# Kernel optimization log

Measured on AMD Instinct MI355X. Metric: run time of the kernel, lower is better.

The kernel has to match this reference:

```python
import jax, jax.numpy as jnp
import numpy as np

N, E, H, C = 10000, 160000, 7, 64
NEG_SLOPE = 0.2


def setup_inputs() -> dict:
    key = jax.random.key(0)
    ks = iter(jax.random.split(key, 32))
    def w(shape, fan_in):
        return jax.random.normal(next(ks), shape, jnp.float32) * (1.0 / np.sqrt(fan_in))
    inp = {
        "x": jax.random.normal(next(ks), (N, 1024), jnp.float32),
        "edge_index": jax.random.randint(next(ks), (2, E), 0, N, jnp.int64),
        # input MLP 1024->512->256->64
        "W1": w((1024, 512), 1024), "b1": jnp.zeros((512,), jnp.float32),
        "W2": w((512, 256), 512),   "b2": jnp.zeros((256,), jnp.float32),
        "W3": w((256, 64), 256),    "b3": jnp.zeros((64,), jnp.float32),
        # 5 stacked GATv2Conv(64,64,heads=7,concat=False) layers
        "Wl": w((5, 64, H * C), 64), "bl": jnp.zeros((5, H * C), jnp.float32),
        "Wr": w((5, 64, H * C), 64),
        "att": w((5, H, C), C),
        "cbias": jnp.zeros((5, C), jnp.float32),
        # output MLP 64->32->16->9
        "V1": w((64, 32), 64), "c1": jnp.zeros((32,), jnp.float32),
        "V2": w((32, 16), 32), "c2": jnp.zeros((16,), jnp.float32),
        "V3": w((16, 9), 16),  "c3": jnp.zeros((9,), jnp.float32),
    }
    return inp


def _gatv2_conv(x, src, dst, Wl, bl, Wr, att, bias):
    # x: [N,64]; src/dst: [E'] (self-loops already appended)
    xl = (x @ Wl + bl).reshape(N, H, C)   # lin_l (with bias)
    xr = (x @ Wr).reshape(N, H, C)        # lin_r (no bias)
    e = jax.nn.leaky_relu(xl[src] + xr[dst], NEG_SLOPE)      # [E',H,C]
    logits = jnp.einsum('ehc,hc->eh', e, att)                # [E',H]
    m = jax.ops.segment_max(logits, dst, num_segments=N)     # [N,H]
    a = jnp.exp(logits - m[dst])
    s = jax.ops.segment_sum(a, dst, num_segments=N)          # [N,H]
    alpha = a / (s[dst] + 1e-16)                             # ragged softmax per dst node
    out = jax.ops.segment_sum(alpha[:, :, None] * xl[src], dst, num_segments=N)  # [N,H,C]
    return out.mean(axis=1) + bias                           # concat=False -> mean heads


def reference(x, edge_index, W1, b1, W2, b2, W3, b3, Wl, bl, Wr, att, cbias,
              V1, c1, V2, c2, V3, c3):
    # GATv2Conv adds self-loops by default
    loops = jnp.arange(N, dtype=edge_index.dtype)
    src = jnp.concatenate([edge_index[0], loops])
    dst = jnp.concatenate([edge_index[1], loops])

    h = jax.nn.relu(x @ W1 + b1)
    h = jax.nn.relu(h @ W2 + b2)
    h = jax.nn.relu(h @ W3 + b3)
    for l in range(5):
        h = jax.nn.relu(_gatv2_conv(h, src, dst, Wl[l], bl[l], Wr[l], att[l], cbias[l]))
    h = jax.nn.relu(h) @ V1 + c1
    h = jax.nn.relu(h) @ V2 + c2
    h = jax.nn.relu(h) @ V3 + c3
    return jax.nn.log_softmax(h, axis=1)
```

## Files before the change

kernel.cpp:

```cpp
#include <hip/hip_runtime.h>
#include <hip/hip_bf16.h>
#include <math.h>

#define NNODES 10000
#define NEDGES 160000
#define ETOT (NEDGES + NNODES)
#define HEADS 7
#define CH 64
#define HC 448
#define HCP 1024

typedef __attribute__((ext_vector_type(8))) short short8;
typedef __attribute__((ext_vector_type(4))) float floatx4;

__device__ __forceinline__ float bf_lo(unsigned u) {
  return __uint_as_float(u << 16);
}
__device__ __forceinline__ float bf_hi(unsigned u) {
  return __uint_as_float(u & 0xffff0000u);
}

__global__ __launch_bounds__(256) void convert_f32_bf16(
    const float* __restrict__ in, short* __restrict__ out, int n4) {
  int i = blockIdx.x * 256 + threadIdx.x;
  if (i < n4) {
    float4 v = *(const float4*)&in[(size_t)i * 4];
    short4 o;
    o.x = __bfloat16_as_short(__float2bfloat16(v.x));
    o.y = __bfloat16_as_short(__float2bfloat16(v.y));
    o.z = __bfloat16_as_short(__float2bfloat16(v.z));
    o.w = __bfloat16_as_short(__float2bfloat16(v.w));
    *(short4*)&out[(size_t)i * 4] = o;
  }
}

__global__ __launch_bounds__(256) void transpose_bf16(
    const float* __restrict__ in, short* __restrict__ out, int K, int N) {
  int idx = blockIdx.x * 256 + threadIdx.x;
  if (idx < K * N) {
    int n = idx / K, k = idx % K;
    out[idx] = __bfloat16_as_short(__float2bfloat16(in[(size_t)k * N + n]));
  }
}

__global__ __launch_bounds__(256) void pack_gat(
    const float* __restrict__ Wl, const float* __restrict__ Wr,
    const float* __restrict__ bl, short* __restrict__ Wgt,
    float* __restrict__ bg) {
  int idx = blockIdx.x * 256 + threadIdx.x;
  if (idx < 5 * HCP * 64) {
    int l = idx / (HCP * 64);
    int rem = idx % (HCP * 64);
    int col = rem / 64, k = rem % 64;
    int half = col >> 9;
    int within = col & 511;
    int c = within >> 3, h = within & 7;
    float v = 0.f;
    if (h < 7) {
      const float* W = half ? Wr : Wl;
      v = W[((size_t)l * 64 + k) * HC + h * 64 + c];
    }
    Wgt[idx] = __bfloat16_as_short(__float2bfloat16(v));
  }
  if (idx < 5 * HCP) {
    int l = idx >> 10, col = idx & 1023;
    int half = col >> 9, within = col & 511;
    int c = within >> 3, h = within & 7;
    bg[idx] = (!half && h < 7) ? bl[(size_t)l * HC + h * 64 + c] : 0.f;
  }
}

template <int BM, int BN, int RELU>
__global__ __launch_bounds__(256) void mfma_gemm(
    const short* __restrict__ A, const short* __restrict__ Bt,
    const float* __restrict__ bias, short* __restrict__ C,
    int M, int K, int Nc) {
  __shared__ short As[BM * 64];
  __shared__ short Bs[BN * 64];
  constexpr int MI = BM / 32;
  constexpr int NJ = BN / 32;
  int tid = threadIdx.x;
  int lane = tid & 63, wave = tid >> 6;
  int wm = wave >> 1, wn = wave & 1;
  int row0 = blockIdx.x * BM, col0 = blockIdx.y * BN;
  floatx4 acc[MI][NJ] = {};

  for (int k0 = 0; k0 < K; k0 += 64) {
    #pragma unroll
    for (int i = 0; i < BM / 32; ++i) {
      int c = i * 4 + wave;
      int r = c * 8 + (lane >> 3);
      int k = (lane & 7) * 8;
      int grow = row0 + r;
      if (grow >= M) grow = M - 1;
      __builtin_amdgcn_global_load_lds(
          (const __attribute__((address_space(1))) void*)(A + (size_t)grow * K + k0 + k),
          (__attribute__((address_space(3))) void*)(As + c * 512), 16, 0, 0);
    }
    #pragma unroll
    for (int i = 0; i < BN / 32; ++i) {
      int c = i * 4 + wave;
      int r = c * 8 + (lane >> 3);
      int k = (lane & 7) * 8;
      int gcol = col0 + r;
      if (gcol >= Nc) gcol = Nc - 1;
      __builtin_amdgcn_global_load_lds(
          (const __attribute__((address_space(1))) void*)(Bt + (size_t)gcol * K + k0 + k),
          (__attribute__((address_space(3))) void*)(Bs + c * 512), 16, 0, 0);
    }
    __syncthreads();
    int lr = lane & 15, lq = lane >> 4;
    #pragma unroll
    for (int kk = 0; kk < 64; kk += 32) {
      short8 af[MI], bf[NJ];
      #pragma unroll
      for (int i = 0; i < MI; ++i)
        af[i] = *(const short8*)&As[(wm * (BM / 2) + i * 16 + lr) * 64 + kk + lq * 8];
      #pragma unroll
      for (int j = 0; j < NJ; ++j)
        bf[j] = *(const short8*)&Bs[(wn * (BN / 2) + j * 16 + lr) * 64 + kk + lq * 8];
      #pragma unroll
      for (int i = 0; i < MI; ++i)
        #pragma unroll
        for (int j = 0; j < NJ; ++j)
          acc[i][j] = __builtin_amdgcn_mfma_f32_16x16x32_bf16(
              af[i], bf[j], acc[i][j], 0, 0, 0);
    }
    __syncthreads();
  }

  int lr = lane & 15, lq = lane >> 4;
  #pragma unroll
  for (int j = 0; j < NJ; ++j) {
    int col = col0 + wn * (BN / 2) + j * 16 + lr;
    float bj = bias ? bias[col] : 0.f;
    #pragma unroll
    for (int i = 0; i < MI; ++i) {
      int rbase = row0 + wm * (BM / 2) + i * 16 + lq * 4;
      #pragma unroll
      for (int r = 0; r < 4; ++r) {
        int row = rbase + r;
        if (row < M) {
          float v = acc[i][j][r] + bj;
          if (RELU) v = fmaxf(v, 0.f);
          C[(size_t)row * Nc + col] = __bfloat16_as_short(__float2bfloat16(v));
        }
      }
    }
  }
}

__global__ void init_cnt(int* __restrict__ cnt) {
  int i = blockIdx.x * 256 + threadIdx.x;
  if (i < NNODES) cnt[i] = 1;
}

__global__ void hist_kernel(const int* __restrict__ ei, int* __restrict__ cnt) {
  int e = blockIdx.x * 256 + threadIdx.x;
  if (e < NEDGES) atomicAdd(&cnt[ei[NEDGES + e]], 1);
}

__global__ __launch_bounds__(1024) void scan_kernel(
    const int* __restrict__ cnt, int* __restrict__ row_start,
    int* __restrict__ cursor) {
  __shared__ int wsum[16];
  int t = threadIdx.x;
  int lane = t & 63, w = t >> 6;
  int base = t * 10;
  int v[10], s = 0;
  #pragma unroll
  for (int i = 0; i < 10; ++i) {
    v[i] = (base + i < NNODES) ? cnt[base + i] : 0;
    s += v[i];
  }
  int incl = s;
  #pragma unroll
  for (int off = 1; off < 64; off <<= 1) {
    int o = __shfl_up(incl, off, 64);
    if (lane >= off) incl += o;
  }
  if (lane == 63) wsum[w] = incl;
  __syncthreads();
  if (w == 0) {
    int wv = (lane < 16) ? wsum[lane] : 0;
    #pragma unroll
    for (int off = 1; off < 16; off <<= 1) {
      int o = __shfl_up(wv, off, 64);
      if (lane >= off) wv += o;
    }
    if (lane < 16) wsum[lane] = wv;
  }
  __syncthreads();
  int woff = (w > 0) ? wsum[w - 1] : 0;
  int excl = woff + incl - s;
  #pragma unroll
  for (int i = 0; i < 10; ++i) {
    if (base + i < NNODES) {
      row_start[base + i] = excl;
      cursor[base + i] = excl;
    }
    excl += v[i];
  }
  if (t == 1023) row_start[NNODES] = wsum[15];
}

__global__ void scatter_self(int* __restrict__ cursor,
                             int* __restrict__ csr_src,
                             int* __restrict__ csr_dst) {
  int n = blockIdx.x * 256 + threadIdx.x;
  if (n < NNODES) {
    int pos = atomicAdd(&cursor[n], 1);
    csr_src[pos] = n;
    csr_dst[pos] = n;
  }
}

__global__ void scatter_kernel(const int* __restrict__ ei,
                               int* __restrict__ cursor,
                               int* __restrict__ csr_src,
                               int* __restrict__ csr_dst) {
  int e = blockIdx.x * 256 + threadIdx.x;
  if (e < NEDGES) {
    int d = ei[NEDGES + e];
    int pos = atomicAdd(&cursor[d], 1);
    csr_src[pos] = ei[e];
    csr_dst[pos] = d;
  }
}

__global__ __launch_bounds__(256) void edge_logits_kernel(
    const short* __restrict__ xlt, const float* __restrict__ att,
    const int* __restrict__ csr_src, const int* __restrict__ csr_dst,
    float* __restrict__ logits) {
  __shared__ float att_s[512];
  for (int i = threadIdx.x; i < 512; i += 256) {
    int c = i >> 3, h = i & 7;
    att_s[i] = (h < 7) ? att[h * 64 + c] : 0.f;
  }
  __syncthreads();
  int lane = threadIdx.x & 63;
  int wid = threadIdx.x >> 6;
  int eo = lane >> 3, cl = lane & 7;
  int e = (blockIdx.x * 4 + wid) * 8 + eo;
  int ec = (e < ETOT) ? e : (ETOT - 1);
  int s = csr_src[ec], d = csr_dst[ec];
  const uint4* xlp = (const uint4*)(xlt + (size_t)s * HCP);
  const uint4* xrp = (const uint4*)(xlt + (size_t)d * HCP + 512);
  float acc[7];
  #pragma unroll
  for (int h = 0; h < 7; ++h) acc[h] = 0.f;
  #pragma unroll
  for (int q = 0; q < 8; ++q) {
    int c = q * 8 + cl;
    uint4 a = xlp[c];
    uint4 b = xrp[c];
    float4 t0 = *(const float4*)&att_s[c * 8];
    float4 t1 = *(const float4*)&att_s[c * 8 + 4];
    float e0 = bf_lo(a.x) + bf_lo(b.x);
    float e1 = bf_hi(a.x) + bf_hi(b.x);
    float e2 = bf_lo(a.y) + bf_lo(b.y);
    float e3 = bf_hi(a.y) + bf_hi(b.y);
    float e4 = bf_lo(a.z) + bf_lo(b.z);
    float e5 = bf_hi(a.z) + bf_hi(b.z);
    float e6 = bf_lo(a.w) + bf_lo(b.w);
    e0 = fmaxf(e0, 0.2f * e0); e1 = fmaxf(e1, 0.2f * e1);
    e2 = fmaxf(e2, 0.2f * e2); e3 = fmaxf(e3, 0.2f * e3);
    e4 = fmaxf(e4, 0.2f * e4); e5 = fmaxf(e5, 0.2f * e5);
    e6 = fmaxf(e6, 0.2f * e6);
    acc[0] += t0.x * e0; acc[1] += t0.y * e1;
    acc[2] += t0.z * e2; acc[3] += t0.w * e3;
    acc[4] += t1.x * e4; acc[5] += t1.y * e5;
    acc[6] += t1.z * e6;
  }
  #pragma unroll
  for (int h = 0; h < 7; ++h) {
    acc[h] += __shfl_xor(acc[h], 1, 64);
    acc[h] += __shfl_xor(acc[h], 2, 64);
    acc[h] += __shfl_xor(acc[h], 4, 64);
  }
  float res = 0.f;
  #pragma unroll
  for (int h = 0; h < 7; ++h) res = (cl == h) ? acc[h] : res;
  if (e < ETOT) logits[(size_t)e * 8 + cl] = res;
}

__global__ __launch_bounds__(256) void gat_agg2_kernel(
    const short* __restrict__ xlt, const float* __restrict__ logits,
    const float* __restrict__ cbias, const int* __restrict__ row_start,
    const int* __restrict__ csr_src, short* __restrict__ hout) {
  __shared__ float alpha_s[4][64];
  int lane = threadIdx.x & 63;
  int wid = threadIdx.x >> 6;
  int n = blockIdx.x * 4 + wid;
  if (n >= NNODES) return;
  int beg = row_start[n], end = row_start[n + 1];

  int eo = lane >> 3, hm = lane & 7;
  float m = -1e30f, ssum = 0.f;
  for (int e = beg + eo; e < end; e += 8) {
    float lg = logits[(size_t)e * 8 + hm];
    float nm = fmaxf(m, lg);
    ssum = ssum * __expf(m - nm) + __expf(lg - nm);
    m = nm;
  }
  #pragma unroll
  for (int st = 8; st <= 32; st <<= 1) {
    float om = __shfl_xor(m, st, 64);
    float os = __shfl_xor(ssum, st, 64);
    float nm = fmaxf(m, om);
    ssum = ssum * __expf(m - nm) + os * __expf(om - nm);
    m = nm;
  }
  float rinv = 1.0f / (ssum + 1e-16f);

  float o0 = 0.f, o1 = 0.f, o2 = 0.f, o3 = 0.f, o4 = 0.f, o5 = 0.f, o6 = 0.f;
  for (int g = beg; g < end; g += 8) {
    int e = g + eo;
    float al = 0.f;
    if (e < end) al = __expf(logits[(size_t)e * 8 + hm] - m) * rinv;
    alpha_s[wid][eo * 8 + hm] = al;
    int lim = end - g;
    if (lim > 8) lim = 8;
    for (int t = 0; t < lim; ++t) {
      int s = csr_src[g + t];
      uint4 xv = *(const uint4*)(xlt + (size_t)s * HCP + lane * 8);
      float4 aA = *(const float4*)&alpha_s[wid][t * 8];
      float4 aB = *(const float4*)&alpha_s[wid][t * 8 + 4];
      o0 += aA.x * bf_lo(xv.x);
      o1 += aA.y * bf_hi(xv.x);
      o2 += aA.z * bf_lo(xv.y);
      o3 += aA.w * bf_hi(xv.y);
      o4 += aB.x * bf_lo(xv.z);
      o5 += aB.y * bf_hi(xv.z);
      o6 += aB.z * bf_lo(xv.w);
    }
  }

  float accv = o0 + o1 + o2 + o3 + o4 + o5 + o6;
  float v = accv * (1.0f / 7.0f) + cbias[lane];
  hout[(size_t)n * 64 + lane] =
      __bfloat16_as_short(__float2bfloat16(fmaxf(v, 0.f)));
}

__global__ __launch_bounds__(256) void out_mlp_kernel(
    const short* __restrict__ h, const float* __restrict__ V1,
    const float* __restrict__ c1, const float* __restrict__ V2,
    const float* __restrict__ c2, const float* __restrict__ V3,
    const float* __restrict__ c3, float* __restrict__ out) {
  __shared__ float hb[4][64], r1[4][32], r2[4][16], z3[4][9];
  int wid = threadIdx.x >> 6;
  int t = threadIdx.x & 63;
  int n = blockIdx.x * 4 + wid;
  hb[wid][t] =
      __uint_as_float(((unsigned)((const unsigned short*)h)[(size_t)n * 64 + t]) << 16);
  __syncthreads();
  if (t < 32) {
    float a = c1[t];
    #pragma unroll
    for (int k = 0; k < 64; ++k) a += hb[wid][k] * V1[k * 32 + t];
    r1[wid][t] = fmaxf(a, 0.f);
  }
  __syncthreads();
  if (t < 16) {
    float a = c2[t];
    #pragma unroll
    for (int k = 0; k < 32; ++k) a += r1[wid][k] * V2[k * 16 + t];
    r2[wid][t] = fmaxf(a, 0.f);
  }
  __syncthreads();
  if (t < 9) {
    float a = c3[t];
    #pragma unroll
    for (int k = 0; k < 16; ++k) a += r2[wid][k] * V3[k * 9 + t];
    z3[wid][t] = a;
  }
  __syncthreads();
  if (t < 9) {
    float mx = z3[wid][0];
    #pragma unroll
    for (int k = 1; k < 9; ++k) mx = fmaxf(mx, z3[wid][k]);
    float s = 0.f;
    #pragma unroll
    for (int k = 0; k < 9; ++k) s += __expf(z3[wid][k] - mx);
    out[(size_t)n * 9 + t] = z3[wid][t] - mx - logf(s);
  }
}

extern "C" void kernel_launch(void* const* d_in, const int* in_sizes, int n_in,
                              void* d_out, int out_size, void* d_ws, size_t ws_size,
                              hipStream_t stream) {
  const float* x   = (const float*)d_in[0];
  const int*   ei  = (const int*)d_in[1];
  const float* W1  = (const float*)d_in[2];
  const float* b1  = (const float*)d_in[3];
  const float* W2  = (const float*)d_in[4];
  const float* b2  = (const float*)d_in[5];
  const float* W3  = (const float*)d_in[6];
  const float* b3  = (const float*)d_in[7];
  const float* Wl  = (const float*)d_in[8];
  const float* bl  = (const float*)d_in[9];
  const float* Wr  = (const float*)d_in[10];
  const float* att = (const float*)d_in[11];
  const float* cb  = (const float*)d_in[12];
  const float* V1  = (const float*)d_in[13];
  const float* c1  = (const float*)d_in[14];
  const float* V2  = (const float*)d_in[15];
  const float* c2  = (const float*)d_in[16];
  const float* V3  = (const float*)d_in[17];
  const float* c3  = (const float*)d_in[18];
  float* out = (float*)d_out;

  char* ws = (char*)d_ws;
  size_t off = 0;
  auto alloc = [&](size_t bytes) {
    void* p = ws + off;
    off = (off + bytes + 255) & ~(size_t)255;
    return p;
  };
  char* region0 = (char*)alloc((size_t)NNODES * 1024 * 2 + 1024);
  short* xb  = (short*)region0;
  short* h2  = (short*)region0;
  short* xlt = (short*)region0;
  char* region1 = (char*)alloc((size_t)NNODES * 512 * 2 + 1024);
  short* h1 = (short*)region1;
  short* hA = (short*)region1;
  short* hB = hA + (size_t)NNODES * 64;
  short* W1t = (short*)alloc((size_t)512 * 1024 * 2);
  short* W2t = (short*)alloc((size_t)256 * 512 * 2);
  short* W3t = (short*)alloc((size_t)64 * 256 * 2);
  short* Wgt = (short*)alloc((size_t)5 * HCP * 64 * 2);
  float* bg  = (float*)alloc((size_t)5 * HCP * 4);
  int* cnt       = (int*)alloc((size_t)NNODES * 4);
  int* row_start = (int*)alloc((size_t)(NNODES + 1) * 4);
  int* cursor    = (int*)alloc((size_t)NNODES * 4);
  int* csr_src   = (int*)alloc((size_t)ETOT * 4);
  int* csr_dst   = (int*)alloc((size_t)ETOT * 4);
  float* logits  = (float*)alloc((size_t)ETOT * 8 * 4);

  convert_f32_bf16<<<(NNODES * 1024 / 4 + 255) / 256, 256, 0, stream>>>(
      x, xb, NNODES * 1024 / 4);
  transpose_bf16<<<(1024 * 512 + 255) / 256, 256, 0, stream>>>(W1, W1t, 1024, 512);
  transpose_bf16<<<(512 * 256 + 255) / 256, 256, 0, stream>>>(W2, W2t, 512, 256);
  transpose_bf16<<<(256 * 64 + 255) / 256, 256, 0, stream>>>(W3, W3t, 256, 64);
  pack_gat<<<(5 * HCP * 64 + 255) / 256, 256, 0, stream>>>(Wl, Wr, bl, Wgt, bg);

  init_cnt<<<(NNODES + 255) / 256, 256, 0, stream>>>(cnt);
  hist_kernel<<<(NEDGES + 255) / 256, 256, 0, stream>>>(ei, cnt);
  scan_kernel<<<1, 1024, 0, stream>>>(cnt, row_start, cursor);
  scatter_self<<<(NNODES + 255) / 256, 256, 0, stream>>>(cursor, csr_src, csr_dst);
  scatter_kernel<<<(NEDGES + 255) / 256, 256, 0, stream>>>(ei, cursor, csr_src, csr_dst);

  mfma_gemm<64, 128, 1><<<dim3(157, 4), 256, 0, stream>>>(
      xb, W1t, b1, h1, NNODES, 1024, 512);
  mfma_gemm<64, 128, 1><<<dim3(157, 2), 256, 0, stream>>>(
      h1, W2t, b2, h2, NNODES, 512, 256);
  mfma_gemm<64, 64, 1><<<dim3(157, 1), 256, 0, stream>>>(
      h2, W3t, b3, hA, NNODES, 256, 64);

  short* hcur = hA;
  short* hnext = hB;
  for (int layer = 0; layer < 5; ++layer) {
    mfma_gemm<128, 128, 0><<<dim3(79, 8), 256, 0, stream>>>(
        hcur, Wgt + (size_t)layer * HCP * 64, bg + (size_t)layer * HCP, xlt,
        NNODES, 64, HCP);
    edge_logits_kernel<<<(ETOT + 31) / 32, 256, 0, stream>>>(
        xlt, att + (size_t)layer * HC, csr_src, csr_dst, logits);
    gat_agg2_kernel<<<2500, 256, 0, stream>>>(
        xlt, logits, cb + (size_t)layer * 64, row_start, csr_src, hnext);
    short* tmp = hcur; hcur = hnext; hnext = tmp;
  }

  out_mlp_kernel<<<2500, 256, 0, stream>>>(hcur, V1, c1, V2, c2, V3, c3, out);
}
```

Before: 576.0 us.

## Fuse GATv2 edge-logit computation into aggregation with online softmax

```diff
diff --git a/kernel.cpp b/kernel.cpp
--- a/kernel.cpp
+++ b/kernel.cpp
@@ -205,125 +205,116 @@
 }
 
 __global__ void scatter_self(int* __restrict__ cursor,
-                             int* __restrict__ csr_src,
-                             int* __restrict__ csr_dst) {
+                             int* __restrict__ csr_src) {
   int n = blockIdx.x * 256 + threadIdx.x;
   if (n < NNODES) {
     int pos = atomicAdd(&cursor[n], 1);
     csr_src[pos] = n;
-    csr_dst[pos] = n;
   }
 }
 
 __global__ void scatter_kernel(const int* __restrict__ ei,
                                int* __restrict__ cursor,
-                               int* __restrict__ csr_src,
-                               int* __restrict__ csr_dst) {
+                               int* __restrict__ csr_src) {
   int e = blockIdx.x * 256 + threadIdx.x;
   if (e < NEDGES) {
     int d = ei[NEDGES + e];
     int pos = atomicAdd(&cursor[d], 1);
     csr_src[pos] = ei[e];
-    csr_dst[pos] = d;
-  }
-}
-
-__global__ __launch_bounds__(256) void edge_logits_kernel(
+  }
+}
+
+__global__ __launch_bounds__(256) void gat_fused_kernel(
     const short* __restrict__ xlt, const float* __restrict__ att,
-    const int* __restrict__ csr_src, const int* __restrict__ csr_dst,
-    float* __restrict__ logits) {
+    const float* __restrict__ cbias, const int* __restrict__ row_start,
+    const int* __restrict__ csr_src, short* __restrict__ hout) {
   __shared__ float att_s[512];
+  __shared__ float alpha_s[4][64];
   for (int i = threadIdx.x; i < 512; i += 256) {
     int c = i >> 3, h = i & 7;
     att_s[i] = (h < 7) ? att[h * 64 + c] : 0.f;
   }
   __syncthreads();
-  int lane = threadIdx.x & 63;
-  int wid = threadIdx.x >> 6;
-  int eo = lane >> 3, cl = lane & 7;
-  int e = (blockIdx.x * 4 + wid) * 8 + eo;
-  int ec = (e < ETOT) ? e : (ETOT - 1);
-  int s = csr_src[ec], d = csr_dst[ec];
-  const uint4* xlp = (const uint4*)(xlt + (size_t)s * HCP);
-  const uint4* xrp = (const uint4*)(xlt + (size_t)d * HCP + 512);
-  float acc[7];
-  #pragma unroll
-  for (int h = 0; h < 7; ++h) acc[h] = 0.f;
-  #pragma unroll
-  for (int q = 0; q < 8; ++q) {
-    int c = q * 8 + cl;
-    uint4 a = xlp[c];
-    uint4 b = xrp[c];
-    float4 t0 = *(const float4*)&att_s[c * 8];
-    float4 t1 = *(const float4*)&att_s[c * 8 + 4];
-    float e0 = bf_lo(a.x) + bf_lo(b.x);
-    float e1 = bf_hi(a.x) + bf_hi(b.x);
-    float e2 = bf_lo(a.y) + bf_lo(b.y);
-    float e3 = bf_hi(a.y) + bf_hi(b.y);
-    float e4 = bf_lo(a.z) + bf_lo(b.z);
-    float e5 = bf_hi(a.z) + bf_hi(b.z);
-    float e6 = bf_lo(a.w) + bf_lo(b.w);
-    e0 = fmaxf(e0, 0.2f * e0); e1 = fmaxf(e1, 0.2f * e1);
-    e2 = fmaxf(e2, 0.2f * e2); e3 = fmaxf(e3, 0.2f * e3);
-    e4 = fmaxf(e4, 0.2f * e4); e5 = fmaxf(e5, 0.2f * e5);
-    e6 = fmaxf(e6, 0.2f * e6);
-    acc[0] += t0.x * e0; acc[1] += t0.y * e1;
-    acc[2] += t0.z * e2; acc[3] += t0.w * e3;
-    acc[4] += t1.x * e4; acc[5] += t1.y * e5;
-    acc[6] += t1.z * e6;
-  }
-  #pragma unroll
-  for (int h = 0; h < 7; ++h) {
-    acc[h] += __shfl_xor(acc[h], 1, 64);
-    acc[h] += __shfl_xor(acc[h], 2, 64);
-    acc[h] += __shfl_xor(acc[h], 4, 64);
-  }
-  float res = 0.f;
-  #pragma unroll
-  for (int h = 0; h < 7; ++h) res = (cl == h) ? acc[h] : res;
-  if (e < ETOT) logits[(size_t)e * 8 + cl] = res;
-}
-
-__global__ __launch_bounds__(256) void gat_agg2_kernel(
-    const short* __restrict__ xlt, const float* __restrict__ logits,
-    const float* __restrict__ cbias, const int* __restrict__ row_start,
-    const int* __restrict__ csr_src, short* __restrict__ hout) {
-  __shared__ float alpha_s[4][64];
   int lane = threadIdx.x & 63;
   int wid = threadIdx.x >> 6;
   int n = blockIdx.x * 4 + wid;
   if (n >= NNODES) return;
   int beg = row_start[n], end = row_start[n + 1];
-
-  int eo = lane >> 3, hm = lane & 7;
-  float m = -1e30f, ssum = 0.f;
-  for (int e = beg + eo; e < end; e += 8) {
-    float lg = logits[(size_t)e * 8 + hm];
-    float nm = fmaxf(m, lg);
-    ssum = ssum * __expf(m - nm) + __expf(lg - nm);
-    m = nm;
-  }
+  int eo = lane >> 3, cl = lane & 7;
+
+  uint4 xr[8];
   #pragma unroll
-  for (int st = 8; st <= 32; st <<= 1) {
-    float om = __shfl_xor(m, st, 64);
-    float os = __shfl_xor(ssum, st, 64);
-    float nm = fmaxf(m, om);
-    ssum = ssum * __expf(m - nm) + os * __expf(om - nm);
-    m = nm;
-  }
-  float rinv = 1.0f / (ssum + 1e-16f);
-
+  for (int q = 0; q < 8; ++q)
+    xr[q] = *(const uint4*)(xlt + (size_t)n * HCP + 512 + (size_t)(q * 8 + cl) * 8);
+
+  float M = -1e30f;
+  float ssum = 0.f;
   float o0 = 0.f, o1 = 0.f, o2 = 0.f, o3 = 0.f, o4 = 0.f, o5 = 0.f, o6 = 0.f;
+
   for (int g = beg; g < end; g += 8) {
-    int e = g + eo;
-    float al = 0.f;
-    if (e < end) al = __expf(logits[(size_t)e * 8 + hm] - m) * rinv;
-    alpha_s[wid][eo * 8 + hm] = al;
     int lim = end - g;
     if (lim > 8) lim = 8;
+    int e = g + eo;
+    int src = csr_src[(e < end) ? e : (end - 1)];
+
+    float a0 = 0.f, a1 = 0.f, a2 = 0.f, a3 = 0.f, a4 = 0.f, a5 = 0.f, a6 = 0.f;
+    const short* xlp = xlt + (size_t)src * HCP;
+    #pragma unroll
+    for (int q = 0; q < 8; ++q) {
+      int c = q * 8 + cl;
+      uint4 a = *(const uint4*)(xlp + (size_t)c * 8);
+      uint4 b = xr[q];
+      float4 t0 = *(const float4*)&att_s[c * 8];
+      float4 t1 = *(const float4*)&att_s[c * 8 + 4];
+      float e0 = bf_lo(a.x) + bf_lo(b.x);
+      float e1 = bf_hi(a.x) + bf_hi(b.x);
+      float e2 = bf_lo(a.y) + bf_lo(b.y);
+      float e3 = bf_hi(a.y) + bf_hi(b.y);
+      float e4 = bf_lo(a.z) + bf_lo(b.z);
+      float e5 = bf_hi(a.z) + bf_hi(b.z);
+      float e6 = bf_lo(a.w) + bf_lo(b.w);
+      e0 = fmaxf(e0, 0.2f * e0); e1 = fmaxf(e1, 0.2f * e1);
+      e2 = fmaxf(e2, 0.2f * e2); e3 = fmaxf(e3, 0.2f * e3);
+      e4 = fmaxf(e4, 0.2f * e4); e5 = fmaxf(e5, 0.2f * e5);
+      e6 = fmaxf(e6, 0.2f * e6);
+      a0 += t0.x * e0; a1 += t0.y * e1;
+      a2 += t0.z * e2; a3 += t0.w * e3;
+      a4 += t1.x * e4; a5 += t1.y * e5;
+      a6 += t1.z * e6;
+    }
+    #pragma unroll
+    for (int st = 1; st <= 4; st <<= 1) {
+      a0 += __shfl_xor(a0, st, 64); a1 += __shfl_xor(a1, st, 64);
+      a2 += __shfl_xor(a2, st, 64); a3 += __shfl_xor(a3, st, 64);
+      a4 += __shfl_xor(a4, st, 64); a5 += __shfl_xor(a5, st, 64);
+      a6 += __shfl_xor(a6, st, 64);
+    }
+    float lg = -1e30f;
+    lg = (cl == 0) ? a0 : lg; lg = (cl == 1) ? a1 : lg;
+    lg = (cl == 2) ? a2 : lg; lg = (cl == 3) ? a3 : lg;
+    lg = (cl == 4) ? a4 : lg; lg = (cl == 5) ? a5 : lg;
+    lg = (cl == 6) ? a6 : lg;
+    if (eo >= lim) lg = -1e30f;
+
+    float cm = lg;
+    cm = fmaxf(cm, __shfl_xor(cm, 8, 64));
+    cm = fmaxf(cm, __shfl_xor(cm, 16, 64));
+    cm = fmaxf(cm, __shfl_xor(cm, 32, 64));
+    float Mn = fmaxf(M, cm);
+    float sc = __expf(M - Mn);
+    float w = __expf(lg - Mn);
+    M = Mn;
+    ssum = ssum * sc + w;
+    alpha_s[wid][eo * 8 + cl] = w;
+    float s0 = __shfl(sc, 0, 64), s1 = __shfl(sc, 1, 64);
+    float s2 = __shfl(sc, 2, 64), s3 = __shfl(sc, 3, 64);
+    float s4 = __shfl(sc, 4, 64), s5 = __shfl(sc, 5, 64);
+    float s6 = __shfl(sc, 6, 64);
+    o0 *= s0; o1 *= s1; o2 *= s2; o3 *= s3; o4 *= s4; o5 *= s5; o6 *= s6;
+
     for (int t = 0; t < lim; ++t) {
-      int s = csr_src[g + t];
-      uint4 xv = *(const uint4*)(xlt + (size_t)s * HCP + lane * 8);
+      int s = __shfl(src, t * 8, 64);
+      uint4 xv = *(const uint4*)(xlt + (size_t)s * HCP + (size_t)lane * 8);
       float4 aA = *(const float4*)&alpha_s[wid][t * 8];
       float4 aB = *(const float4*)&alpha_s[wid][t * 8 + 4];
       o0 += aA.x * bf_lo(xv.x);
@@ -336,7 +327,15 @@
     }
   }
 
-  float accv = o0 + o1 + o2 + o3 + o4 + o5 + o6;
+  ssum += __shfl_xor(ssum, 8, 64);
+  ssum += __shfl_xor(ssum, 16, 64);
+  ssum += __shfl_xor(ssum, 32, 64);
+  float rinv = 1.0f / (ssum + 1e-16f);
+  float r0 = __shfl(rinv, 0, 64), r1 = __shfl(rinv, 1, 64);
+  float r2 = __shfl(rinv, 2, 64), r3 = __shfl(rinv, 3, 64);
+  float r4 = __shfl(rinv, 4, 64), r5 = __shfl(rinv, 5, 64);
+  float r6 = __shfl(rinv, 6, 64);
+  float accv = o0 * r0 + o1 * r1 + o2 * r2 + o3 * r3 + o4 * r4 + o5 * r5 + o6 * r6;
   float v = accv * (1.0f / 7.0f) + cbias[lane];
   hout[(size_t)n * 64 + lane] =
       __bfloat16_as_short(__float2bfloat16(fmaxf(v, 0.f)));
@@ -434,8 +433,6 @@
   int* row_start = (int*)alloc((size_t)(NNODES + 1) * 4);
   int* cursor    = (int*)alloc((size_t)NNODES * 4);
   int* csr_src   = (int*)alloc((size_t)ETOT * 4);
-  int* csr_dst   = (int*)alloc((size_t)ETOT * 4);
-  float* logits  = (float*)alloc((size_t)ETOT * 8 * 4);
 
   convert_f32_bf16<<<(NNODES * 1024 / 4 + 255) / 256, 256, 0, stream>>>(
       x, xb, NNODES * 1024 / 4);
@@ -447,8 +444,8 @@
   init_cnt<<<(NNODES + 255) / 256, 256, 0, stream>>>(cnt);
   hist_kernel<<<(NEDGES + 255) / 256, 256, 0, stream>>>(ei, cnt);
   scan_kernel<<<1, 1024, 0, stream>>>(cnt, row_start, cursor);
-  scatter_self<<<(NNODES + 255) / 256, 256, 0, stream>>>(cursor, csr_src, csr_dst);
-  scatter_kernel<<<(NEDGES + 255) / 256, 256, 0, stream>>>(ei, cursor, csr_src, csr_dst);
+  scatter_self<<<(NNODES + 255) / 256, 256, 0, stream>>>(cursor, csr_src);
+  scatter_kernel<<<(NEDGES + 255) / 256, 256, 0, stream>>>(ei, cursor, csr_src);
 
   mfma_gemm<64, 128, 1><<<dim3(157, 4), 256, 0, stream>>>(
       xb, W1t, b1, h1, NNODES, 1024, 512);
@@ -463,10 +460,9 @@
     mfma_gemm<128, 128, 0><<<dim3(79, 8), 256, 0, stream>>>(
         hcur, Wgt + (size_t)layer * HCP * 64, bg + (size_t)layer * HCP, xlt,
         NNODES, 64, HCP);
-    edge_logits_kernel<<<(ETOT + 31) / 32, 256, 0, stream>>>(
-        xlt, att + (size_t)layer * HC, csr_src, csr_dst, logits);
-    gat_agg2_kernel<<<2500, 256, 0, stream>>>(
-        xlt, logits, cb + (size_t)layer * 64, row_start, csr_src, hnext);
+    gat_fused_kernel<<<2500, 256, 0, stream>>>(
+        xlt, att + (size_t)layer * HC, cb + (size_t)layer * 64,
+        row_start, csr_src, hnext);
     short* tmp = hcur; hcur = hnext; hnext = tmp;
   }
 
```

Result: slower. 661.7 us (+14.9%).

## Drop max-subtraction in softmax, exponentiate logits in edge kernel and fuse normalization

Applied to the files above, without the earlier changes.

```diff
diff --git a/kernel.cpp b/kernel.cpp
--- a/kernel.cpp
+++ b/kernel.cpp
@@ -231,7 +231,7 @@
 __global__ __launch_bounds__(256) void edge_logits_kernel(
     const short* __restrict__ xlt, const float* __restrict__ att,
     const int* __restrict__ csr_src, const int* __restrict__ csr_dst,
-    float* __restrict__ logits) {
+    float* __restrict__ wbuf) {
   __shared__ float att_s[512];
   for (int i = threadIdx.x; i < 512; i += 256) {
     int c = i >> 3, h = i & 7;
@@ -281,62 +281,42 @@
   float res = 0.f;
   #pragma unroll
   for (int h = 0; h < 7; ++h) res = (cl == h) ? acc[h] : res;
-  if (e < ETOT) logits[(size_t)e * 8 + cl] = res;
+  float wv = (cl < 7) ? __expf(res) : 0.f;
+  if (e < ETOT) wbuf[(size_t)e * 8 + cl] = wv;
 }
 
 __global__ __launch_bounds__(256) void gat_agg2_kernel(
-    const short* __restrict__ xlt, const float* __restrict__ logits,
+    const short* __restrict__ xlt, const float* __restrict__ wbuf,
     const float* __restrict__ cbias, const int* __restrict__ row_start,
     const int* __restrict__ csr_src, short* __restrict__ hout) {
-  __shared__ float alpha_s[4][64];
   int lane = threadIdx.x & 63;
   int wid = threadIdx.x >> 6;
   int n = blockIdx.x * 4 + wid;
   if (n >= NNODES) return;
   int beg = row_start[n], end = row_start[n + 1];
 
-  int eo = lane >> 3, hm = lane & 7;
-  float m = -1e30f, ssum = 0.f;
-  for (int e = beg + eo; e < end; e += 8) {
-    float lg = logits[(size_t)e * 8 + hm];
-    float nm = fmaxf(m, lg);
-    ssum = ssum * __expf(m - nm) + __expf(lg - nm);
-    m = nm;
-  }
-  #pragma unroll
-  for (int st = 8; st <= 32; st <<= 1) {
-    float om = __shfl_xor(m, st, 64);
-    float os = __shfl_xor(ssum, st, 64);
-    float nm = fmaxf(m, om);
-    ssum = ssum * __expf(m - nm) + os * __expf(om - nm);
-    m = nm;
-  }
-  float rinv = 1.0f / (ssum + 1e-16f);
-
   float o0 = 0.f, o1 = 0.f, o2 = 0.f, o3 = 0.f, o4 = 0.f, o5 = 0.f, o6 = 0.f;
-  for (int g = beg; g < end; g += 8) {
-    int e = g + eo;
-    float al = 0.f;
-    if (e < end) al = __expf(logits[(size_t)e * 8 + hm] - m) * rinv;
-    alpha_s[wid][eo * 8 + hm] = al;
-    int lim = end - g;
-    if (lim > 8) lim = 8;
-    for (int t = 0; t < lim; ++t) {
-      int s = csr_src[g + t];
-      uint4 xv = *(const uint4*)(xlt + (size_t)s * HCP + lane * 8);
-      float4 aA = *(const float4*)&alpha_s[wid][t * 8];
-      float4 aB = *(const float4*)&alpha_s[wid][t * 8 + 4];
-      o0 += aA.x * bf_lo(xv.x);
-      o1 += aA.y * bf_hi(xv.x);
-      o2 += aA.z * bf_lo(xv.y);
-      o3 += aA.w * bf_hi(xv.y);
-      o4 += aB.x * bf_lo(xv.z);
-      o5 += aB.y * bf_hi(xv.z);
-      o6 += aB.z * bf_lo(xv.w);
-    }
-  }
-
-  float accv = o0 + o1 + o2 + o3 + o4 + o5 + o6;
+  float s0 = 0.f, s1 = 0.f, s2 = 0.f, s3 = 0.f, s4 = 0.f, s5 = 0.f, s6 = 0.f;
+  #pragma unroll 2
+  for (int e = beg; e < end; ++e) {
+    int src = csr_src[e];
+    float4 wa = *(const float4*)&wbuf[(size_t)e * 8];
+    float4 wb = *(const float4*)&wbuf[(size_t)e * 8 + 4];
+    uint4 xv = *(const uint4*)(xlt + (size_t)src * HCP + (size_t)lane * 8);
+    o0 += wa.x * bf_lo(xv.x);
+    o1 += wa.y * bf_hi(xv.x);
+    o2 += wa.z * bf_lo(xv.y);
+    o3 += wa.w * bf_hi(xv.y);
+    o4 += wb.x * bf_lo(xv.z);
+    o5 += wb.y * bf_hi(xv.z);
+    o6 += wb.z * bf_lo(xv.w);
+    s0 += wa.x; s1 += wa.y; s2 += wa.z; s3 += wa.w;
+    s4 += wb.x; s5 += wb.y; s6 += wb.z;
+  }
+
+  float accv = o0 / (s0 + 1e-16f) + o1 / (s1 + 1e-16f) + o2 / (s2 + 1e-16f) +
+               o3 / (s3 + 1e-16f) + o4 / (s4 + 1e-16f) + o5 / (s5 + 1e-16f) +
+               o6 / (s6 + 1e-16f);
   float v = accv * (1.0f / 7.0f) + cbias[lane];
   hout[(size_t)n * 64 + lane] =
       __bfloat16_as_short(__float2bfloat16(fmaxf(v, 0.f)));
@@ -435,7 +415,7 @@
   int* cursor    = (int*)alloc((size_t)NNODES * 4);
   int* csr_src   = (int*)alloc((size_t)ETOT * 4);
   int* csr_dst   = (int*)alloc((size_t)ETOT * 4);
-  float* logits  = (float*)alloc((size_t)ETOT * 8 * 4);
+  float* wbuf    = (float*)alloc((size_t)ETOT * 8 * 4);
 
   convert_f32_bf16<<<(NNODES * 1024 / 4 + 255) / 256, 256, 0, stream>>>(
       x, xb, NNODES * 1024 / 4);
@@ -464,9 +444,9 @@
         hcur, Wgt + (size_t)layer * HCP * 64, bg + (size_t)layer * HCP, xlt,
         NNODES, 64, HCP);
     edge_logits_kernel<<<(ETOT + 31) / 32, 256, 0, stream>>>(
-        xlt, att + (size_t)layer * HC, csr_src, csr_dst, logits);
+        xlt, att + (size_t)layer * HC, csr_src, csr_dst, wbuf);
     gat_agg2_kernel<<<2500, 256, 0, stream>>>(
-        xlt, logits, cb + (size_t)layer * 64, row_start, csr_src, hnext);
+        xlt, wbuf, cb + (size_t)layer * 64, row_start, csr_src, hnext);
     short* tmp = hcur; hcur = hnext; hnext = tmp;
   }
 
```

Result: no change. 579.8 us (+0.6%).
